# Performance work log

Hardware: AMD Instinct MI355X
Metric: run time of the kernel (lower is better)

Reference implementation:

```python
import jax, jax.numpy as jnp
import numpy as np

N_NODES = 1024  # cities (fully connected graph)
N_HID = 128     # config.N: edge-MLP hidden dim (W2: N_HID x 3)
M = 128         # config.M: embedding dim
T = 4           # config.T: message-passing iterations
TAU = 10.0      # config.tau: softmax temperature


def setup_inputs() -> dict:
    key = jax.random.key(0)
    ks = jax.random.split(key, 18)
    u = lambda k, s: jax.random.uniform(k, s, dtype=jnp.float32)
    return dict(
        D=u(ks[0], (N_NODES, N_NODES)),       # pairwise distances graph[v][u]
        dd=u(ks[1], (N_NODES,)),              # graph[depot][v]
        dr=u(ks[2], (N_NODES,)),              # distance_from_robot()
        ddep=u(ks[3], (N_NODES,)),            # distance_from_depot()
        mu0_A1=u(ks[4], (N_NODES, M)),
        mu0_A2=u(ks[5], (N_NODES, M)),
        mu0_B=u(ks[6], (N_NODES, M)),
        W1=u(ks[7], (1, N_HID)),
        W2=u(ks[8], (N_HID, 3)),
        W3_A1=u(ks[9], (M, M + 1)),
        W3_A2=u(ks[10], (M, M + 1)),
        W4_A1=u(ks[11], (M, 1)),
        W4_A2=u(ks[12], (M, 1)),
        W3_B=u(ks[13], (M, M)),
        W4_B=u(ks[14], (M, 2 * M)),
        W5=u(ks[15], (1, M)),
        W6=u(ks[16], (1, M)),
        W7=u(ks[17], (1, M)),
    )


def _edge_scores(D, dd, W1, W2):
    # G[v,u] = W1 @ relu(W2 @ [D[v,u], dd[v], dd[u]])  -> scalar per pair
    h = (D[:, :, None] * W2[:, 0]
         + dd[:, None, None] * W2[:, 1]
         + dd[None, :, None] * W2[:, 2])            # (n, n, N_HID)
    return jnp.maximum(h, 0.0) @ W1[0]              # (n, n)


def _attn(G):
    # p[u,v] = softmax over sources u != v of G[u,v]/tau
    n = G.shape[0]
    Gm = jnp.where(jnp.eye(n, dtype=bool), -jnp.inf, G / TAU)
    return jax.nn.softmax(Gm, axis=0)


def _layer_A(P, wd, mu, Wg, W3, W4, dist):
    # l_v = [ sum_u p_uv * D[u,v] * relu(Wg @ mu_v) ; sum_u p_uv * mu_u ]
    # mu_v <- relu(W3 @ l_v + W4 * dist_v)
    for _ in range(T):
        s = jnp.maximum(mu @ Wg[0], 0.0)                        # (n,)
        l = jnp.concatenate([(wd * s)[:, None], P.T @ mu], 1)   # (n, M+1)
        mu = jnp.maximum(l @ W3.T + dist[:, None] * W4[:, 0][None, :], 0.0)
    return mu


def reference(D, dd, dr, ddep, mu0_A1, mu0_A2, mu0_B,
              W1, W2, W3_A1, W3_A2, W4_A1, W4_A2, W3_B, W4_B, W5, W6, W7):
    # A1 and B use distances / 1000 for edge scores; A2 uses raw distances.
    G_scaled = _edge_scores(D / 1000.0, dd / 1000.0, W1, W2)
    G_raw = _edge_scores(D, dd, W1, W2)
    P1 = _attn(G_scaled)
    P2 = _attn(G_raw)
    wd1 = jnp.sum(P1 * D, axis=0)   # attention-weighted raw edge distance, per v
    wd2 = jnp.sum(P2 * D, axis=0)

    A1 = _layer_A(P1, wd1, mu0_A1, W5, W3_A1, W4_A1, dr)
    A2 = _layer_A(P2, wd2, mu0_A2, W6, W3_A2, W4_A2, ddep)

    bias = jnp.concatenate([A1, A2], axis=1) @ W4_B.T  # (n, M), constant over t
    mu = mu0_B
    for _ in range(T):
        mu = jnp.maximum((P1.T @ mu) @ W3_B.T + bias, 0.0)

    return jnp.maximum(W7 @ jnp.sum(mu, axis=0)[:, None], 0.0)  # (1, 1)
```

## Files before the change

### kernel.cpp

```cpp
#include <hip/hip_runtime.h>
#include <math.h>

#define N 1024
#define M 128

__global__ __launch_bounds__(256) void k_prep(const float* __restrict__ D, float* __restrict__ DT,
    const float* __restrict__ W3A1, const float* __restrict__ W3A2,
    const float* __restrict__ W3B, const float* __restrict__ W4B,
    float* __restrict__ oA1, float* __restrict__ oA2,
    float* __restrict__ oB, float* __restrict__ o4B,
    float* __restrict__ gsum, unsigned int* __restrict__ gcnt) {
  int bx = blockIdx.x, t = threadIdx.x;
  if (bx < 1024) {
    __shared__ float tile[32 * 33];
    int tx = t & 31, ty = t >> 5;
    int bxx = (bx & 31) * 32, by = (bx >> 5) * 32;
#pragma unroll
    for (int i = 0; i < 4; i++)
      tile[(ty + i * 8) * 33 + tx] = D[(size_t)(by + ty + i * 8) * N + bxx + tx];
    __syncthreads();
#pragma unroll
    for (int i = 0; i < 4; i++)
      DT[(size_t)(bxx + ty + i * 8) * N + by + tx] = tile[tx * 33 + ty + i * 8];
  } else if (bx < 1345) {
    int idx = (bx - 1024) * 256 + t;
    const float* in = nullptr; float* op = nullptr; int cols = 0, o = 0;
    if (idx < 16512)      { in = W3A1; op = oA1; cols = 129; o = idx; }
    else if (idx < 33024) { in = W3A2; op = oA2; cols = 129; o = idx - 16512; }
    else if (idx < 49408) { in = W3B;  op = oB;  cols = 128; o = idx - 33024; }
    else if (idx < 82176) { in = W4B;  op = o4B; cols = 256; o = idx - 49408; }
    if (in) { int r = o & 127, c = o >> 7; op[o] = in[r * cols + c]; }
  } else {
    if (t == 0) { *gsum = 0.f; *gcnt = 0u; }
  }
}

__device__ __forceinline__ float blk_max(float v, float* red, int t) {
#pragma unroll
  for (int o = 32; o; o >>= 1) v = fmaxf(v, __shfl_xor(v, o));
  __syncthreads();
  if ((t & 63) == 0) red[t >> 6] = v;
  __syncthreads();
  return fmaxf(fmaxf(red[0], red[1]), fmaxf(red[2], red[3]));
}
__device__ __forceinline__ float blk_sum(float v, float* red, int t) {
#pragma unroll
  for (int o = 32; o; o >>= 1) v += __shfl_xor(v, o);
  __syncthreads();
  if ((t & 63) == 0) red[t >> 6] = v;
  __syncthreads();
  return red[0] + red[1] + red[2] + red[3];
}

__global__ __launch_bounds__(256) void k_edge(const float* __restrict__ DT,
                                              const float* __restrict__ dd,
                                              const float* __restrict__ W1,
                                              const float* __restrict__ W2,
                                              float* __restrict__ PT1, float* __restrict__ PT2,
                                              float* __restrict__ wd1, float* __restrict__ wd2) {
  __shared__ float4 wp[128];
  __shared__ float red[4];
  int t = threadIdx.x, v = blockIdx.x;
  if (t < 128) {
    float4 p;
    p.x = W2[t * 3 + 0]; p.y = W2[t * 3 + 1]; p.z = W2[t * 3 + 2]; p.w = W1[t];
    wp[t] = p;
  }
  __syncthreads();
  float yv = dd[v];
  float x[4], z[4], g[4] = {0.f, 0.f, 0.f, 0.f};
#pragma unroll
  for (int i = 0; i < 4; i++) {
    int u = t + i * 256;
    x[i] = DT[(size_t)v * N + u];
    z[i] = dd[u];
  }
#pragma unroll 2
  for (int k = 0; k < 128; k++) {
    float4 wk = wp[k];
    float cv = yv * wk.z;
#pragma unroll
    for (int i = 0; i < 4; i++) {
      float h = fmaf(x[i], wk.x, fmaf(z[i], wk.y, cv));
      g[i] = fmaf(fmaxf(h, 0.f), wk.w, g[i]);
    }
  }
#pragma unroll
  for (int i = 0; i < 4; i++)
    if (t + i * 256 == v) g[i] = -INFINITY;
  float m = fmaxf(fmaxf(g[0], g[1]), fmaxf(g[2], g[3]));
  m = blk_max(m, red, t);
  float er[4], es[4], sr = 0.f, ss = 0.f;
#pragma unroll
  for (int i = 0; i < 4; i++) {
    er[i] = expf((g[i] - m) * 0.1f);
    es[i] = expf((g[i] - m) * 1e-4f);
    sr += er[i]; ss += es[i];
  }
  sr = blk_sum(sr, red, t);
  ss = blk_sum(ss, red, t);
  float ir = 1.f / sr, is = 1.f / ss;
  float a1 = 0.f, a2 = 0.f;
#pragma unroll
  for (int i = 0; i < 4; i++) {
    int u = t + i * 256;
    float pr = er[i] * ir, ps = es[i] * is;
    PT2[(size_t)v * N + u] = pr;
    PT1[(size_t)v * N + u] = ps;
    a1 += ps * x[i];
    a2 += pr * x[i];
  }
  a1 = blk_sum(a1, red, t);
  a2 = blk_sum(a2, red, t);
  if (t == 0) { wd1[v] = a1; wd2[v] = a2; }
}

__device__ __forceinline__ void gemm4(const float* __restrict__ PT,
                                      const float* __restrict__ cur,
                                      float* __restrict__ As, float* __restrict__ CsP,
                                      int r0, int t) {
#pragma unroll
  for (int i = 0; i < 4; i++) {
    int idx = t + i * 256;
    int row = idx >> 8, c4 = idx & 255;
    ((float4*)As)[row * 256 + c4] = *((const float4*)(PT + (size_t)(r0 + row) * N) + c4);
  }
  __syncthreads();
  const int kc = t >> 5;
  const int cg = t & 31;
  const int u0 = kc * 128;
  float4 acc0 = {0,0,0,0}, acc1 = {0,0,0,0}, acc2 = {0,0,0,0}, acc3 = {0,0,0,0};
  const float* mub = cur + (size_t)u0 * M + cg * 4;
  const float* a0p = As + u0;
  const float* a1p = As + 1024 + u0;
  const float* a2p = As + 2048 + u0;
  const float* a3p = As + 3072 + u0;
#pragma unroll 2
  for (int uu = 0; uu < 128; uu += 4) {
    float4 a0 = *(const float4*)&a0p[uu];
    float4 a1 = *(const float4*)&a1p[uu];
    float4 a2 = *(const float4*)&a2p[uu];
    float4 a3 = *(const float4*)&a3p[uu];
    float4 b0 = *(const float4*)&mub[(size_t)(uu + 0) * M];
    float4 b1 = *(const float4*)&mub[(size_t)(uu + 1) * M];
    float4 b2 = *(const float4*)&mub[(size_t)(uu + 2) * M];
    float4 b3 = *(const float4*)&mub[(size_t)(uu + 3) * M];
#define FMA4(ACC, AV) \
    ACC.x = fmaf(AV.x, b0.x, ACC.x); ACC.y = fmaf(AV.x, b0.y, ACC.y); \
    ACC.z = fmaf(AV.x, b0.z, ACC.z); ACC.w = fmaf(AV.x, b0.w, ACC.w); \
    ACC.x = fmaf(AV.y, b1.x, ACC.x); ACC.y = fmaf(AV.y, b1.y, ACC.y); \
    ACC.z = fmaf(AV.y, b1.z, ACC.z); ACC.w = fmaf(AV.y, b1.w, ACC.w); \
    ACC.x = fmaf(AV.z, b2.x, ACC.x); ACC.y = fmaf(AV.z, b2.y, ACC.y); \
    ACC.z = fmaf(AV.z, b2.z, ACC.z); ACC.w = fmaf(AV.z, b2.w, ACC.w); \
    ACC.x = fmaf(AV.w, b3.x, ACC.x); ACC.y = fmaf(AV.w, b3.y, ACC.y); \
    ACC.z = fmaf(AV.w, b3.z, ACC.z); ACC.w = fmaf(AV.w, b3.w, ACC.w);
    FMA4(acc0, a0) FMA4(acc1, a1) FMA4(acc2, a2) FMA4(acc3, a3)
#undef FMA4
  }
  float* cp = CsP + kc * 512 + cg * 4;
  *(float4*)&cp[0]   = acc0;
  *(float4*)&cp[128] = acc1;
  *(float4*)&cp[256] = acc2;
  *(float4*)&cp[384] = acc3;
  __syncthreads();
#pragma unroll
  for (int i = 0; i < 2; i++) {
    int j = t + i * 256;
    float s = 0.f;
#pragma unroll
    for (int s8 = 0; s8 < 8; s8++) s += CsP[s8 * 512 + j];
    As[j] = s;
  }
}

__global__ __launch_bounds__(256) void k_iterA(
    const float* __restrict__ PT1, const float* __restrict__ PT2,
    const float* __restrict__ cur1, const float* __restrict__ cur2,
    float* __restrict__ nxt1, float* __restrict__ nxt2,
    const float* __restrict__ wd1, const float* __restrict__ wd2,
    const float* __restrict__ dr, const float* __restrict__ ddep,
    const float* __restrict__ W3A1T, const float* __restrict__ W3A2T,
    const float* __restrict__ W4A1, const float* __restrict__ W4A2,
    const float* __restrict__ W5, const float* __restrict__ W6) {
  __shared__ float smem[4096 + 4096 + 4];
  float* As = smem;
  float* CsP = smem + 4096;
  float* swd = smem + 8192;
  int z = blockIdx.z;
  const float* PT = z ? PT2 : PT1;
  const float* cur = z ? cur2 : cur1;
  float* nxt = z ? nxt2 : nxt1;
  const float* wdv = z ? wd2 : wd1;
  const float* dist = z ? ddep : dr;
  const float* W3T = z ? W3A2T : W3A1T;
  const float* W4c = z ? W4A2 : W4A1;
  const float* Wg = z ? W6 : W5;
  int t = threadIdx.x, r0 = blockIdx.x * 4;

  gemm4(PT, cur, As, CsP, r0, t);
  {
    int row = t >> 6, l = t & 63;
    const float* mo = cur + (size_t)(r0 + row) * M;
    float sp = fmaf(mo[l], Wg[l], mo[l + 64] * Wg[l + 64]);
#pragma unroll
    for (int o = 32; o; o >>= 1) sp += __shfl_xor(sp, o);
    if (l == 0) swd[row] = wdv[r0 + row] * fmaxf(sp, 0.f);
  }
  __syncthreads();
  float* Cred = As;

  int col = t & 127, ra = t >> 7;
  float accA = 0.f, accB = 0.f;
  const float* wcol = W3T + 128 + col;
#pragma unroll 4
  for (int m = 0; m < 128; m += 4) {
    float4 c0 = *(const float4*)&Cred[ra * 128 + m];
    float4 c1 = *(const float4*)&Cred[(ra + 2) * 128 + m];
    float w0 = wcol[(m + 0) * 128], w1 = wcol[(m + 1) * 128];
    float w2 = wcol[(m + 2) * 128], w3 = wcol[(m + 3) * 128];
    accA = fmaf(c0.x, w0, fmaf(c0.y, w1, fmaf(c0.z, w2, fmaf(c0.w, w3, accA))));
    accB = fmaf(c1.x, w0, fmaf(c1.y, w1, fmaf(c1.z, w2, fmaf(c1.w, w3, accB))));
  }
  float w30 = W3T[col], w4 = W4c[col];
  float o0 = fmaxf(fmaf(swd[ra], w30, fmaf(dist[r0 + ra], w4, accA)), 0.f);
  float o1 = fmaxf(fmaf(swd[ra + 2], w30, fmaf(dist[r0 + ra + 2], w4, accB)), 0.f);
  nxt[(size_t)(r0 + ra) * M + col] = o0;
  nxt[(size_t)(r0 + ra + 2) * M + col] = o1;
}

__global__ __launch_bounds__(256) void k_iterB(
    const float* __restrict__ PT1, const float* __restrict__ cur, float* __restrict__ nxt,
    const float* __restrict__ W3BT, const float* __restrict__ W4BT, float* __restrict__ biasb,
    const float* __restrict__ A1f, const float* __restrict__ A2f,
    const float* __restrict__ W7, float* __restrict__ gsum, unsigned int* __restrict__ gcnt,
    float* __restrict__ out, int flags) {
  __shared__ float smem[4096 + 4096 + 4];
  float* As = smem;
  float* CsP = smem + 4096;
  float* red = smem + 8192;
  int t = threadIdx.x, r0 = blockIdx.x * 4;

  gemm4(PT1, cur, As, CsP, r0, t);
  __syncthreads();
  float* Cred = As;

  int col = t & 127, ra = t >> 7;
  float bv0, bv1;
  if (flags & 1) {
    bv0 = 0.f; bv1 = 0.f;
    const float* a1a = A1f + (size_t)(r0 + ra) * M;
    const float* a1b = A1f + (size_t)(r0 + ra + 2) * M;
#pragma unroll 4
    for (int c = 0; c < 128; c++) {
      float wv = W4BT[c * 128 + col];
      bv0 = fmaf(a1a[c], wv, bv0);
      bv1 = fmaf(a1b[c], wv, bv1);
    }
    const float* a2a = A2f + (size_t)(r0 + ra) * M;
    const float* a2b = A2f + (size_t)(r0 + ra + 2) * M;
#pragma unroll 4
    for (int c = 0; c < 128; c++) {
      float wv = W4BT[(c + 128) * 128 + col];
      bv0 = fmaf(a2a[c], wv, bv0);
      bv1 = fmaf(a2b[c], wv, bv1);
    }
    biasb[(size_t)(r0 + ra) * M + col] = bv0;
    biasb[(size_t)(r0 + ra + 2) * M + col] = bv1;
  } else {
    bv0 = biasb[(size_t)(r0 + ra) * M + col];
    bv1 = biasb[(size_t)(r0 + ra + 2) * M + col];
  }

  float accA = 0.f, accB = 0.f;
  const float* wcol = W3BT + col;
#pragma unroll 4
  for (int m = 0; m < 128; m += 4) {
    float4 c0 = *(const float4*)&Cred[ra * 128 + m];
    float4 c1 = *(const float4*)&Cred[(ra + 2) * 128 + m];
    float w0 = wcol[(m + 0) * 128], w1 = wcol[(m + 1) * 128];
    float w2 = wcol[(m + 2) * 128], w3 = wcol[(m + 3) * 128];
    accA = fmaf(c0.x, w0, fmaf(c0.y, w1, fmaf(c0.z, w2, fmaf(c0.w, w3, accA))));
    accB = fmaf(c1.x, w0, fmaf(c1.y, w1, fmaf(c1.z, w2, fmaf(c1.w, w3, accB))));
  }
  float o0 = fmaxf(accA + bv0, 0.f);
  float o1 = fmaxf(accB + bv1, 0.f);

  if (!(flags & 2)) {
    nxt[(size_t)(r0 + ra) * M + col] = o0;
    nxt[(size_t)(r0 + ra + 2) * M + col] = o1;
  } else {
    float s = (o0 + o1) * W7[col];
#pragma unroll
    for (int off = 32; off; off >>= 1) s += __shfl_xor(s, off);
    __syncthreads();
    if ((t & 63) == 0) red[t >> 6] = s;
    __syncthreads();
    if (t == 0) {
      float bs = red[0] + red[1] + red[2] + red[3];
      atomicAdd(gsum, bs);
      __threadfence();
      unsigned int old = atomicAdd(gcnt, 1u);
      if (old == 255u) {
        float tot = atomicAdd(gsum, 0.f);
        out[0] = fmaxf(tot, 0.f);
      }
    }
  }
}

extern "C" void kernel_launch(void* const* d_in, const int* in_sizes, int n_in,
                              void* d_out, int out_size, void* d_ws, size_t ws_size,
                              hipStream_t stream) {
  (void)in_sizes; (void)n_in; (void)out_size; (void)ws_size;
  const float* D     = (const float*)d_in[0];
  const float* dd    = (const float*)d_in[1];
  const float* dr    = (const float*)d_in[2];
  const float* ddep  = (const float*)d_in[3];
  const float* mu0A1 = (const float*)d_in[4];
  const float* mu0A2 = (const float*)d_in[5];
  const float* mu0B  = (const float*)d_in[6];
  const float* W1    = (const float*)d_in[7];
  const float* W2    = (const float*)d_in[8];
  const float* W3A1  = (const float*)d_in[9];
  const float* W3A2  = (const float*)d_in[10];
  const float* W4A1  = (const float*)d_in[11];
  const float* W4A2  = (const float*)d_in[12];
  const float* W3B   = (const float*)d_in[13];
  const float* W4B   = (const float*)d_in[14];
  const float* W5    = (const float*)d_in[15];
  const float* W6    = (const float*)d_in[16];
  const float* W7    = (const float*)d_in[17];

  float* w = (float*)d_ws;
  size_t o = 0;
  auto alloc = [&](size_t n) { float* p = w + o; o += n; return p; };
  float* DT    = alloc((size_t)N * N);
  float* PT1   = alloc((size_t)N * N);
  float* PT2   = alloc((size_t)N * N);
  float* wd1   = alloc(N);
  float* wd2   = alloc(N);
  float* W3A1T = alloc(129 * 128);
  float* W3A2T = alloc(129 * 128);
  float* W3BT  = alloc(128 * 128);
  float* W4BT  = alloc(256 * 128);
  float* muA1a = alloc((size_t)N * M); float* muA1b = alloc((size_t)N * M);
  float* muA2a = alloc((size_t)N * M); float* muA2b = alloc((size_t)N * M);
  float* muBa  = alloc((size_t)N * M); float* muBb  = alloc((size_t)N * M);
  float* biasb = alloc((size_t)N * M);
  float* gsum  = alloc(1);
  unsigned int* gcnt = (unsigned int*)alloc(1);

  k_prep<<<1346, 256, 0, stream>>>(D, DT, W3A1, W3A2, W3B, W4B,
                                   W3A1T, W3A2T, W3BT, W4BT, gsum, gcnt);
  k_edge<<<N, 256, 0, stream>>>(DT, dd, W1, W2, PT1, PT2, wd1, wd2);

  const float* c1 = mu0A1;
  const float* c2 = mu0A2;
  float* b1[2] = {muA1a, muA1b};
  float* b2[2] = {muA2a, muA2b};
  for (int it = 0; it < 4; it++) {
    k_iterA<<<dim3(256, 1, 2), 256, 0, stream>>>(PT1, PT2, c1, c2,
        b1[it & 1], b2[it & 1], wd1, wd2, dr, ddep,
        W3A1T, W3A2T, W4A1, W4A2, W5, W6);
    c1 = b1[it & 1];
    c2 = b2[it & 1];
  }

  const float* cB = mu0B;
  float* bB[2] = {muBa, muBb};
  for (int it = 0; it < 4; it++) {
    int flags = (it == 0 ? 1 : 0) | (it == 3 ? 2 : 0);
    k_iterB<<<256, 256, 0, stream>>>(PT1, cB, bB[it & 1],
        W3BT, W4BT, biasb, muA1b, muA2b,
        W7, gsum, gcnt, (float*)d_out, flags);
    cB = bB[it & 1];
  }
}
```

Baseline: 158.6 us.

## Store attention and embeddings in bf16, fuse first B iteration into A pass

```diff
diff --git a/kernel.cpp b/kernel.cpp
--- a/kernel.cpp
+++ b/kernel.cpp
@@ -4,11 +4,28 @@
 #define N 1024
 #define M 128
 
-__global__ __launch_bounds__(256) void k_prep(const float* __restrict__ D, float* __restrict__ DT,
+typedef unsigned short us16;
+
+__device__ __forceinline__ us16 f2bf(float f) {
+  unsigned int u = __float_as_uint(f);
+  unsigned int r = u + 0x7FFFu + ((u >> 16) & 1u);
+  return (us16)(r >> 16);
+}
+__device__ __forceinline__ float bf2f(us16 u) {
+  return __uint_as_float(((unsigned int)u) << 16);
+}
+
+__global__ __launch_bounds__(256) void k_prep(
+    const float* __restrict__ D, float* __restrict__ DT,
     const float* __restrict__ W3A1, const float* __restrict__ W3A2,
     const float* __restrict__ W3B, const float* __restrict__ W4B,
-    float* __restrict__ oA1, float* __restrict__ oA2,
-    float* __restrict__ oB, float* __restrict__ o4B,
+    float* __restrict__ W3A1T, float* __restrict__ W3A2T,
+    float* __restrict__ W3BT, float* __restrict__ W4BT,
+    const float* __restrict__ mu0A1, const float* __restrict__ mu0A2,
+    const float* __restrict__ mu0B,
+    const float* __restrict__ W5, const float* __restrict__ W6,
+    float* __restrict__ s1, float* __restrict__ s2,
+    us16* __restrict__ muA1_0, us16* __restrict__ muA2_0, us16* __restrict__ muB_0,
     float* __restrict__ gsum, unsigned int* __restrict__ gcnt) {
   int bx = blockIdx.x, t = threadIdx.x;
   if (bx < 1024) {
@@ -25,11 +42,35 @@
   } else if (bx < 1345) {
     int idx = (bx - 1024) * 256 + t;
     const float* in = nullptr; float* op = nullptr; int cols = 0, o = 0;
-    if (idx < 16512)      { in = W3A1; op = oA1; cols = 129; o = idx; }
-    else if (idx < 33024) { in = W3A2; op = oA2; cols = 129; o = idx - 16512; }
-    else if (idx < 49408) { in = W3B;  op = oB;  cols = 128; o = idx - 33024; }
-    else if (idx < 82176) { in = W4B;  op = o4B; cols = 256; o = idx - 49408; }
+    if (idx < 16512)      { in = W3A1; op = W3A1T; cols = 129; o = idx; }
+    else if (idx < 33024) { in = W3A2; op = W3A2T; cols = 129; o = idx - 16512; }
+    else if (idx < 49408) { in = W3B;  op = W3BT;  cols = 128; o = idx - 33024; }
+    else if (idx < 82176) { in = W4B;  op = W4BT;  cols = 256; o = idx - 49408; }
     if (in) { int r = o & 127, c = o >> 7; op[o] = in[r * cols + c]; }
+  } else if (bx < 1473) {
+    int idx = (bx - 1345) * 256 + t;
+    int row = idx >> 4, l16 = idx & 15;
+    int chain = row >> 10, r = row & 1023;
+    const float* mu0 = chain ? mu0A2 : mu0A1;
+    const float* Wg = chain ? W6 : W5;
+    float* sb = chain ? s2 : s1;
+    const float* mp = mu0 + (size_t)r * M + l16 * 8;
+    float4 a0 = *(const float4*)mp, a1 = *(const float4*)(mp + 4);
+    float4 g0 = *(const float4*)(Wg + l16 * 8), g1 = *(const float4*)(Wg + l16 * 8 + 4);
+    float sp = a0.x * g0.x + a0.y * g0.y + a0.z * g0.z + a0.w * g0.w
+             + a1.x * g1.x + a1.y * g1.y + a1.z * g1.z + a1.w * g1.w;
+#pragma unroll
+    for (int o = 8; o; o >>= 1) sp += __shfl_xor(sp, o);
+    if (l16 == 0) sb[r] = sp;
+  } else if (bx < 1857) {
+    int idx = (bx - 1473) * 256 + t;
+    int mat = idx >> 15, o4 = idx & 32767;
+    const float* src = mat == 0 ? mu0A1 : (mat == 1 ? mu0A2 : mu0B);
+    us16* dst = mat == 0 ? muA1_0 : (mat == 1 ? muA2_0 : muB_0);
+    float4 v = *(const float4*)(src + (size_t)o4 * 4);
+    ushort4 p;
+    p.x = f2bf(v.x); p.y = f2bf(v.y); p.z = f2bf(v.z); p.w = f2bf(v.w);
+    *(ushort4*)(dst + (size_t)o4 * 4) = p;
   } else {
     if (t == 0) { *gsum = 0.f; *gcnt = 0u; }
   }
@@ -56,7 +97,7 @@
                                               const float* __restrict__ dd,
                                               const float* __restrict__ W1,
                                               const float* __restrict__ W2,
-                                              float* __restrict__ PT1, float* __restrict__ PT2,
+                                              us16* __restrict__ PT1bf, us16* __restrict__ PT2bf,
                                               float* __restrict__ wd1, float* __restrict__ wd2) {
   __shared__ float4 wp[128];
   __shared__ float red[4];
@@ -68,13 +109,11 @@
   }
   __syncthreads();
   float yv = dd[v];
-  float x[4], z[4], g[4] = {0.f, 0.f, 0.f, 0.f};
-#pragma unroll
-  for (int i = 0; i < 4; i++) {
-    int u = t + i * 256;
-    x[i] = DT[(size_t)v * N + u];
-    z[i] = dd[u];
-  }
+  float4 xv = *(const float4*)&DT[(size_t)v * N + t * 4];
+  float4 zv = *(const float4*)&dd[t * 4];
+  float x[4] = {xv.x, xv.y, xv.z, xv.w};
+  float z[4] = {zv.x, zv.y, zv.z, zv.w};
+  float g[4] = {0.f, 0.f, 0.f, 0.f};
 #pragma unroll 2
   for (int k = 0; k < 128; k++) {
     float4 wk = wp[k];
@@ -87,7 +126,7 @@
   }
 #pragma unroll
   for (int i = 0; i < 4; i++)
-    if (t + i * 256 == v) g[i] = -INFINITY;
+    if (t * 4 + i == v) g[i] = -INFINITY;
   float m = fmaxf(fmaxf(g[0], g[1]), fmaxf(g[2], g[3]));
   m = blk_max(m, red, t);
   float er[4], es[4], sr = 0.f, ss = 0.f;
@@ -100,37 +139,39 @@
   sr = blk_sum(sr, red, t);
   ss = blk_sum(ss, red, t);
   float ir = 1.f / sr, is = 1.f / ss;
-  float a1 = 0.f, a2 = 0.f;
-#pragma unroll
-  for (int i = 0; i < 4; i++) {
-    int u = t + i * 256;
-    float pr = er[i] * ir, ps = es[i] * is;
-    PT2[(size_t)v * N + u] = pr;
-    PT1[(size_t)v * N + u] = ps;
-    a1 += ps * x[i];
-    a2 += pr * x[i];
-  }
+  float ps0 = es[0] * is, ps1 = es[1] * is, ps2 = es[2] * is, ps3 = es[3] * is;
+  float pr0 = er[0] * ir, pr1 = er[1] * ir, pr2 = er[2] * ir, pr3 = er[3] * ir;
+  ushort4 p1, p2;
+  p1.x = f2bf(ps0); p1.y = f2bf(ps1); p1.z = f2bf(ps2); p1.w = f2bf(ps3);
+  p2.x = f2bf(pr0); p2.y = f2bf(pr1); p2.z = f2bf(pr2); p2.w = f2bf(pr3);
+  *(ushort4*)(PT1bf + (size_t)v * N + t * 4) = p1;
+  *(ushort4*)(PT2bf + (size_t)v * N + t * 4) = p2;
+  float a1 = ps0 * x[0] + ps1 * x[1] + ps2 * x[2] + ps3 * x[3];
+  float a2 = pr0 * x[0] + pr1 * x[1] + pr2 * x[2] + pr3 * x[3];
   a1 = blk_sum(a1, red, t);
   a2 = blk_sum(a2, red, t);
   if (t == 0) { wd1[v] = a1; wd2[v] = a2; }
 }
 
-__device__ __forceinline__ void gemm4(const float* __restrict__ PT,
-                                      const float* __restrict__ cur,
-                                      float* __restrict__ As, float* __restrict__ CsP,
-                                      int r0, int t) {
+__device__ __forceinline__ void gemm4_bf(const us16* __restrict__ PTbf,
+                                         const us16* __restrict__ curbf,
+                                         float* __restrict__ As, float* __restrict__ CsP,
+                                         int r0, int t) {
 #pragma unroll
   for (int i = 0; i < 4; i++) {
     int idx = t + i * 256;
     int row = idx >> 8, c4 = idx & 255;
-    ((float4*)As)[row * 256 + c4] = *((const float4*)(PT + (size_t)(r0 + row) * N) + c4);
+    ushort4 a = *(const ushort4*)(PTbf + (size_t)(r0 + row) * N + c4 * 4);
+    float4 f;
+    f.x = bf2f(a.x); f.y = bf2f(a.y); f.z = bf2f(a.z); f.w = bf2f(a.w);
+    *(float4*)&As[row * 1024 + c4 * 4] = f;
   }
   __syncthreads();
   const int kc = t >> 5;
   const int cg = t & 31;
   const int u0 = kc * 128;
   float4 acc0 = {0,0,0,0}, acc1 = {0,0,0,0}, acc2 = {0,0,0,0}, acc3 = {0,0,0,0};
-  const float* mub = cur + (size_t)u0 * M + cg * 4;
+  const us16* mub = curbf + (size_t)u0 * M + cg * 4;
   const float* a0p = As + u0;
   const float* a1p = As + 1024 + u0;
   const float* a2p = As + 2048 + u0;
@@ -141,10 +182,14 @@
     float4 a1 = *(const float4*)&a1p[uu];
     float4 a2 = *(const float4*)&a2p[uu];
     float4 a3 = *(const float4*)&a3p[uu];
-    float4 b0 = *(const float4*)&mub[(size_t)(uu + 0) * M];
-    float4 b1 = *(const float4*)&mub[(size_t)(uu + 1) * M];
-    float4 b2 = *(const float4*)&mub[(size_t)(uu + 2) * M];
-    float4 b3 = *(const float4*)&mub[(size_t)(uu + 3) * M];
+    ushort4 v0 = *(const ushort4*)&mub[(size_t)(uu + 0) * M];
+    ushort4 v1 = *(const ushort4*)&mub[(size_t)(uu + 1) * M];
+    ushort4 v2 = *(const ushort4*)&mub[(size_t)(uu + 2) * M];
+    ushort4 v3 = *(const ushort4*)&mub[(size_t)(uu + 3) * M];
+    float4 b0 = {bf2f(v0.x), bf2f(v0.y), bf2f(v0.z), bf2f(v0.w)};
+    float4 b1 = {bf2f(v1.x), bf2f(v1.y), bf2f(v1.z), bf2f(v1.w)};
+    float4 b2 = {bf2f(v2.x), bf2f(v2.y), bf2f(v2.z), bf2f(v2.w)};
+    float4 b3 = {bf2f(v3.x), bf2f(v3.y), bf2f(v3.z), bf2f(v3.w)};
 #define FMA4(ACC, AV) \
     ACC.x = fmaf(AV.x, b0.x, ACC.x); ACC.y = fmaf(AV.x, b0.y, ACC.y); \
     ACC.z = fmaf(AV.x, b0.z, ACC.z); ACC.w = fmaf(AV.x, b0.w, ACC.w); \
@@ -171,132 +216,148 @@
     for (int s8 = 0; s8 < 8; s8++) s += CsP[s8 * 512 + j];
     As[j] = s;
   }
+  __syncthreads();
 }
 
 __global__ __launch_bounds__(256) void k_iterA(
-    const float* __restrict__ PT1, const float* __restrict__ PT2,
-    const float* __restrict__ cur1, const float* __restrict__ cur2,
-    float* __restrict__ nxt1, float* __restrict__ nxt2,
+    const us16* __restrict__ PT1bf, const us16* __restrict__ PT2bf,
+    const us16* __restrict__ cur1, const us16* __restrict__ cur2,
+    const us16* __restrict__ curB0,
+    us16* __restrict__ nxt1, us16* __restrict__ nxt2, float* __restrict__ CB0f,
+    float* __restrict__ s1buf, float* __restrict__ s2buf,
     const float* __restrict__ wd1, const float* __restrict__ wd2,
     const float* __restrict__ dr, const float* __restrict__ ddep,
     const float* __restrict__ W3A1T, const float* __restrict__ W3A2T,
+    const float* __restrict__ W3BT,
     const float* __restrict__ W4A1, const float* __restrict__ W4A2,
     const float* __restrict__ W5, const float* __restrict__ W6) {
-  __shared__ float smem[4096 + 4096 + 4];
+  __shared__ float smem[8192];
   float* As = smem;
   float* CsP = smem + 4096;
-  float* swd = smem + 8192;
-  int z = blockIdx.z;
-  const float* PT = z ? PT2 : PT1;
-  const float* cur = z ? cur2 : cur1;
-  float* nxt = z ? nxt2 : nxt1;
-  const float* wdv = z ? wd2 : wd1;
-  const float* dist = z ? ddep : dr;
-  const float* W3T = z ? W3A2T : W3A1T;
-  const float* W4c = z ? W4A2 : W4A1;
-  const float* Wg = z ? W6 : W5;
-  int t = threadIdx.x, r0 = blockIdx.x * 4;
-
-  gemm4(PT, cur, As, CsP, r0, t);
-  {
-    int row = t >> 6, l = t & 63;
-    const float* mo = cur + (size_t)(r0 + row) * M;
-    float sp = fmaf(mo[l], Wg[l], mo[l + 64] * Wg[l + 64]);
-#pragma unroll
-    for (int o = 32; o; o >>= 1) sp += __shfl_xor(sp, o);
-    if (l == 0) swd[row] = wdv[r0 + row] * fmaxf(sp, 0.f);
-  }
-  __syncthreads();
-  float* Cred = As;
-
+  const int z = blockIdx.z;
+  const int t = threadIdx.x, r0 = blockIdx.x * 4;
+  const us16* PT = (z == 1) ? PT2bf : PT1bf;
+  const us16* cur = (z == 0) ? cur1 : (z == 1) ? cur2 : curB0;
+
+  gemm4_bf(PT, cur, As, CsP, r0, t);
+
+  const float* W3T = (z == 0) ? W3A1T : (z == 1) ? W3A2T : W3BT;
   int col = t & 127, ra = t >> 7;
   float accA = 0.f, accB = 0.f;
-  const float* wcol = W3T + 128 + col;
+  const float* wcol = W3T + (z < 2 ? 128 : 0) + col;
 #pragma unroll 4
   for (int m = 0; m < 128; m += 4) {
-    float4 c0 = *(const float4*)&Cred[ra * 128 + m];
-    float4 c1 = *(const float4*)&Cred[(ra + 2) * 128 + m];
+    float4 c0 = *(const float4*)&As[ra * 128 + m];
+    float4 c1 = *(const float4*)&As[(ra + 2) * 128 + m];
     float w0 = wcol[(m + 0) * 128], w1 = wcol[(m + 1) * 128];
     float w2 = wcol[(m + 2) * 128], w3 = wcol[(m + 3) * 128];
     accA = fmaf(c0.x, w0, fmaf(c0.y, w1, fmaf(c0.z, w2, fmaf(c0.w, w3, accA))));
     accB = fmaf(c1.x, w0, fmaf(c1.y, w1, fmaf(c1.z, w2, fmaf(c1.w, w3, accB))));
   }
+  int rA = r0 + ra, rB = r0 + ra + 2;
+  if (z == 2) {
+    CB0f[(size_t)rA * M + col] = accA;
+    CB0f[(size_t)rB * M + col] = accB;
+    return;
+  }
+  float* sbuf = z ? s2buf : s1buf;
+  const float* wdv = z ? wd2 : wd1;
+  const float* dist = z ? ddep : dr;
+  const float* W4c = z ? W4A2 : W4A1;
+  const float* Wg = z ? W6 : W5;
+  us16* nxt = z ? nxt2 : nxt1;
   float w30 = W3T[col], w4 = W4c[col];
-  float o0 = fmaxf(fmaf(swd[ra], w30, fmaf(dist[r0 + ra], w4, accA)), 0.f);
-  float o1 = fmaxf(fmaf(swd[ra + 2], w30, fmaf(dist[r0 + ra + 2], w4, accB)), 0.f);
-  nxt[(size_t)(r0 + ra) * M + col] = o0;
-  nxt[(size_t)(r0 + ra + 2) * M + col] = o1;
+  float svA = wdv[rA] * fmaxf(sbuf[rA], 0.f);
+  float svB = wdv[rB] * fmaxf(sbuf[rB], 0.f);
+  float o0 = fmaxf(fmaf(svA, w30, fmaf(dist[rA], w4, accA)), 0.f);
+  float o1 = fmaxf(fmaf(svB, w30, fmaf(dist[rB], w4, accB)), 0.f);
+  nxt[(size_t)rA * M + col] = f2bf(o0);
+  nxt[(size_t)rB * M + col] = f2bf(o1);
+  __syncthreads();
+  CsP[ra * 128 + col] = o0;
+  CsP[(ra + 2) * 128 + col] = o1;
+  __syncthreads();
+  if (t < 64) {
+    int row = t >> 4, l16 = t & 15;
+    const float* cr = &CsP[row * 128 + l16 * 8];
+    float4 x0 = *(const float4*)cr, x1 = *(const float4*)(cr + 4);
+    float4 g0 = *(const float4*)(Wg + l16 * 8), g1 = *(const float4*)(Wg + l16 * 8 + 4);
+    float sp = x0.x * g0.x + x0.y * g0.y + x0.z * g0.z + x0.w * g0.w
+             + x1.x * g1.x + x1.y * g1.y + x1.z * g1.z + x1.w * g1.w;
+#pragma unroll
+    for (int o = 8; o; o >>= 1) sp += __shfl_xor(sp, o);
+    if (l16 == 0) sbuf[r0 + row] = sp;
+  }
+}
+
+__global__ __launch_bounds__(256) void k_bmerge(
+    const us16* __restrict__ A1bf, const us16* __restrict__ A2bf,
+    const float* __restrict__ W4BT, const float* __restrict__ CB0f,
+    float* __restrict__ biasb, us16* __restrict__ muB1) {
+  int t = threadIdx.x, r0 = blockIdx.x * 4;
+  int col = t & 127, ra = t >> 7;
+  int rA = r0 + ra, rB = r0 + ra + 2;
+  float b0 = 0.f, b1 = 0.f;
+  const us16* a1a = A1bf + (size_t)rA * M;
+  const us16* a1b = A1bf + (size_t)rB * M;
+  const us16* a2a = A2bf + (size_t)rA * M;
+  const us16* a2b = A2bf + (size_t)rB * M;
+#pragma unroll 4
+  for (int c = 0; c < 128; c++) {
+    float wv = W4BT[c * 128 + col];
+    b0 = fmaf(bf2f(a1a[c]), wv, b0);
+    b1 = fmaf(bf2f(a1b[c]), wv, b1);
+  }
+#pragma unroll 4
+  for (int c = 0; c < 128; c++) {
+    float wv = W4BT[(c + 128) * 128 + col];
+    b0 = fmaf(bf2f(a2a[c]), wv, b0);
+    b1 = fmaf(bf2f(a2b[c]), wv, b1);
+  }
+  biasb[(size_t)rA * M + col] = b0;
+  biasb[(size_t)rB * M + col] = b1;
+  muB1[(size_t)rA * M + col] = f2bf(fmaxf(CB0f[(size_t)rA * M + col] + b0, 0.f));
+  muB1[(size_t)rB * M + col] = f2bf(fmaxf(CB0f[(size_t)rB * M + col] + b1, 0.f));
 }
 
 __global__ __launch_bounds__(256) void k_iterB(
-    const float* __restrict__ PT1, const float* __restrict__ cur, float* __restrict__ nxt,
-    const float* __restrict__ W3BT, const float* __restrict__ W4BT, float* __restrict__ biasb,
-    const float* __restrict__ A1f, const float* __restrict__ A2f,
-    const float* __restrict__ W7, float* __restrict__ gsum, unsigned int* __restrict__ gcnt,
-    float* __restrict__ out, int flags) {
-  __shared__ float smem[4096 + 4096 + 4];
+    const us16* __restrict__ PT1bf, const us16* __restrict__ curbf,
+    us16* __restrict__ nxtbf,
+    const float* __restrict__ W3BT, const float* __restrict__ biasb,
+    const float* __restrict__ W7, float* __restrict__ gsum,
+    unsigned int* __restrict__ gcnt, float* __restrict__ out, int last) {
+  __shared__ float smem[8192];
+  __shared__ float redf[4];
   float* As = smem;
   float* CsP = smem + 4096;
-  float* red = smem + 8192;
   int t = threadIdx.x, r0 = blockIdx.x * 4;
-
-  gemm4(PT1, cur, As, CsP, r0, t);
-  __syncthreads();
-  float* Cred = As;
-
+  gemm4_bf(PT1bf, curbf, As, CsP, r0, t);
   int col = t & 127, ra = t >> 7;
-  float bv0, bv1;
-  if (flags & 1) {
-    bv0 = 0.f; bv1 = 0.f;
-    const float* a1a = A1f + (size_t)(r0 + ra) * M;
-    const float* a1b = A1f + (size_t)(r0 + ra + 2) * M;
-#pragma unroll 4
-    for (int c = 0; c < 128; c++) {
-      float wv = W4BT[c * 128 + col];
-      bv0 = fmaf(a1a[c], wv, bv0);
-      bv1 = fmaf(a1b[c], wv, bv1);
-    }
-    const float* a2a = A2f + (size_t)(r0 + ra) * M;
-    const float* a2b = A2f + (size_t)(r0 + ra + 2) * M;
-#pragma unroll 4
-    for (int c = 0; c < 128; c++) {
-      float wv = W4BT[(c + 128) * 128 + col];
-      bv0 = fmaf(a2a[c], wv, bv0);
-      bv1 = fmaf(a2b[c], wv, bv1);
-    }
-    biasb[(size_t)(r0 + ra) * M + col] = bv0;
-    biasb[(size_t)(r0 + ra + 2) * M + col] = bv1;
-  } else {
-    bv0 = biasb[(size_t)(r0 + ra) * M + col];
-    bv1 = biasb[(size_t)(r0 + ra + 2) * M + col];
-  }
-
   float accA = 0.f, accB = 0.f;
   const float* wcol = W3BT + col;
 #pragma unroll 4
   for (int m = 0; m < 128; m += 4) {
-    float4 c0 = *(const float4*)&Cred[ra * 128 + m];
-    float4 c1 = *(const float4*)&Cred[(ra + 2) * 128 + m];
+    float4 c0 = *(const float4*)&As[ra * 128 + m];
+    float4 c1 = *(const float4*)&As[(ra + 2) * 128 + m];
     float w0 = wcol[(m + 0) * 128], w1 = wcol[(m + 1) * 128];
     float w2 = wcol[(m + 2) * 128], w3 = wcol[(m + 3) * 128];
     accA = fmaf(c0.x, w0, fmaf(c0.y, w1, fmaf(c0.z, w2, fmaf(c0.w, w3, accA))));
     accB = fmaf(c1.x, w0, fmaf(c1.y, w1, fmaf(c1.z, w2, fmaf(c1.w, w3, accB))));
   }
-  float o0 = fmaxf(accA + bv0, 0.f);
-  float o1 = fmaxf(accB + bv1, 0.f);
-
-  if (!(flags & 2)) {
-    nxt[(size_t)(r0 + ra) * M + col] = o0;
-    nxt[(size_t)(r0 + ra + 2) * M + col] = o1;
+  int rA = r0 + ra, rB = r0 + ra + 2;
+  float o0 = fmaxf(accA + biasb[(size_t)rA * M + col], 0.f);
+  float o1 = fmaxf(accB + biasb[(size_t)rB * M + col], 0.f);
+  if (!last) {
+    nxtbf[(size_t)rA * M + col] = f2bf(o0);
+    nxtbf[(size_t)rB * M + col] = f2bf(o1);
   } else {
     float s = (o0 + o1) * W7[col];
 #pragma unroll
     for (int off = 32; off; off >>= 1) s += __shfl_xor(s, off);
-    __syncthreads();
-    if ((t & 63) == 0) red[t >> 6] = s;
+    if ((t & 63) == 0) redf[t >> 6] = s;
     __syncthreads();
     if (t == 0) {
-      float bs = red[0] + red[1] + red[2] + red[3];
+      float bs = redf[0] + redf[1] + redf[2] + redf[3];
       atomicAdd(gsum, bs);
       __threadfence();
       unsigned int old = atomicAdd(gcnt, 1u);
@@ -331,48 +392,60 @@
   const float* W6    = (const float*)d_in[16];
   const float* W7    = (const float*)d_in[17];
 
-  float* w = (float*)d_ws;
+  float* wsf = (float*)d_ws;
   size_t o = 0;
-  auto alloc = [&](size_t n) { float* p = w + o; o += n; return p; };
-  float* DT    = alloc((size_t)N * N);
-  float* PT1   = alloc((size_t)N * N);
-  float* PT2   = alloc((size_t)N * N);
-  float* wd1   = alloc(N);
-  float* wd2   = alloc(N);
-  float* W3A1T = alloc(129 * 128);
-  float* W3A2T = alloc(129 * 128);
-  float* W3BT  = alloc(128 * 128);
-  float* W4BT  = alloc(256 * 128);
-  float* muA1a = alloc((size_t)N * M); float* muA1b = alloc((size_t)N * M);
-  float* muA2a = alloc((size_t)N * M); float* muA2b = alloc((size_t)N * M);
-  float* muBa  = alloc((size_t)N * M); float* muBb  = alloc((size_t)N * M);
-  float* biasb = alloc((size_t)N * M);
-  float* gsum  = alloc(1);
+  auto alloc = [&](size_t n) { float* p = wsf + o; o += n; return p; };
+  float* DT     = alloc((size_t)N * N);
+  us16* PT1bf   = (us16*)alloc((size_t)N * N / 2);
+  us16* PT2bf   = (us16*)alloc((size_t)N * N / 2);
+  float* W3A1T  = alloc(129 * 128);
+  float* W3A2T  = alloc(129 * 128);
+  float* W3BT   = alloc(128 * 128);
+  float* W4BT   = alloc(256 * 128);
+  float* s1     = alloc(N);
+  float* s2     = alloc(N);
+  float* wd1    = alloc(N);
+  float* wd2    = alloc(N);
+  us16* muA1_0  = (us16*)alloc((size_t)N * M / 2);
+  us16* muA1_a  = (us16*)alloc((size_t)N * M / 2);
+  us16* muA1_b  = (us16*)alloc((size_t)N * M / 2);
+  us16* muA2_0  = (us16*)alloc((size_t)N * M / 2);
+  us16* muA2_a  = (us16*)alloc((size_t)N * M / 2);
+  us16* muA2_b  = (us16*)alloc((size_t)N * M / 2);
+  us16* muB_0   = (us16*)alloc((size_t)N * M / 2);
+  us16* muB_a   = (us16*)alloc((size_t)N * M / 2);
+  us16* muB_b   = (us16*)alloc((size_t)N * M / 2);
+  float* CB0f   = alloc((size_t)N * M);
+  float* biasb  = alloc((size_t)N * M);
+  float* gsum   = alloc(1);
   unsigned int* gcnt = (unsigned int*)alloc(1);
 
-  k_prep<<<1346, 256, 0, stream>>>(D, DT, W3A1, W3A2, W3B, W4B,
-                                   W3A1T, W3A2T, W3BT, W4BT, gsum, gcnt);
-  k_edge<<<N, 256, 0, stream>>>(DT, dd, W1, W2, PT1, PT2, wd1, wd2);
-
-  const float* c1 = mu0A1;
-  const float* c2 = mu0A2;
-  float* b1[2] = {muA1a, muA1b};
-  float* b2[2] = {muA2a, muA2b};
+  k_prep<<<1858, 256, 0, stream>>>(D, DT, W3A1, W3A2, W3B, W4B,
+                                   W3A1T, W3A2T, W3BT, W4BT,
+                                   mu0A1, mu0A2, mu0B, W5, W6, s1, s2,
+                                   muA1_0, muA2_0, muB_0, gsum, gcnt);
+  k_edge<<<N, 256, 0, stream>>>(DT, dd, W1, W2, PT1bf, PT2bf, wd1, wd2);
+
+  const us16* c1 = muA1_0;
+  const us16* c2 = muA2_0;
+  us16* b1[2] = {muA1_a, muA1_b};
+  us16* b2[2] = {muA2_a, muA2_b};
   for (int it = 0; it < 4; it++) {
-    k_iterA<<<dim3(256, 1, 2), 256, 0, stream>>>(PT1, PT2, c1, c2,
-        b1[it & 1], b2[it & 1], wd1, wd2, dr, ddep,
-        W3A1T, W3A2T, W4A1, W4A2, W5, W6);
+    dim3 grid(256, 1, it == 0 ? 3 : 2);
+    k_iterA<<<grid, 256, 0, stream>>>(PT1bf, PT2bf, c1, c2, muB_0,
+        b1[it & 1], b2[it & 1], CB0f, s1, s2, wd1, wd2, dr, ddep,
+        W3A1T, W3A2T, W3BT, W4A1, W4A2, W5, W6);
     c1 = b1[it & 1];
     c2 = b2[it & 1];
   }
 
-  const float* cB = mu0B;
-  float* bB[2] = {muBa, muBb};
-  for (int it = 0; it < 4; it++) {
-    int flags = (it == 0 ? 1 : 0) | (it == 3 ? 2 : 0);
-    k_iterB<<<256, 256, 0, stream>>>(PT1, cB, bB[it & 1],
-        W3BT, W4BT, biasb, muA1b, muA2b,
-        W7, gsum, gcnt, (float*)d_out, flags);
-    cB = bB[it & 1];
-  }
-}
+  k_bmerge<<<256, 256, 0, stream>>>(muA1_b, muA2_b, W4BT, CB0f, biasb, muB_a);
+
+  const us16* cB = muB_a;
+  us16* bB[2] = {muB_b, muB_a};
+  for (int i = 0; i < 3; i++) {
+    k_iterB<<<256, 256, 0, stream>>>(PT1bf, cB, bB[i & 1],
+        W3BT, biasb, W7, gsum, gcnt, (float*)d_out, i == 2 ? 1 : 0);
+    cB = bB[i & 1];
+  }
+}
```

Result: faster. 152.3 us (-4.0%).
